# Optimization experiments

Hardware: AMD Instinct MI355X
Metric: run time of the kernel (lower is better)

## Reference

```python
import jax, jax.numpy as jnp
import numpy as np

DIRECTIONS = [(0, 0), (1, 0), (-1, 0), (0, 1), (0, -1)]  # (dx, dy)
BN_EPS = 1e-5


def shift2d(x, directions=DIRECTIONS):
    # x: (B, C, H, W). Split channels into G groups, roll each spatially,
    # zero out the wrapped-around border (zero_pad mode), then concat.
    C = x.shape[1]
    G = len(directions)
    base = C // G
    sizes = [base] * (G - 1) + [C - base * (G - 1)]
    starts = np.concatenate([[0], np.cumsum(sizes)])
    out = []
    for i, (dx, dy) in enumerate(directions):
        chunk = x[:, starts[i]:starts[i + 1]]
        if dx == 0 and dy == 0:
            out.append(chunk)
            continue
        y = jnp.roll(chunk, shift=(dy, dx), axis=(-2, -1))
        if dy > 0:
            y = y.at[..., :dy, :].set(0.0)
        elif dy < 0:
            y = y.at[..., dy:, :].set(0.0)
        if dx > 0:
            y = y.at[..., :, :dx].set(0.0)
        elif dx < 0:
            y = y.at[..., :, dx:].set(0.0)
        out.append(y)
    return jnp.concatenate(out, axis=1)


def setup_inputs() -> dict:
    key = jax.random.key(0)
    k1, k2, k3, k4 = jax.random.split(key, 4)
    B, Cin, Cout, H, W = 32, 256, 256, 56, 56
    x = jax.random.normal(k1, (B, Cin, H, W), dtype=jnp.float32)
    pw_w = jax.random.normal(k2, (Cout, Cin), dtype=jnp.float32) * (1.0 / np.sqrt(Cin))
    gamma = jnp.ones((Cout,), dtype=jnp.float32)
    beta = jnp.zeros((Cout,), dtype=jnp.float32)
    running_mean = jax.random.normal(k3, (Cout,), dtype=jnp.float32) * 0.1
    running_var = jax.random.uniform(k4, (Cout,), dtype=jnp.float32, minval=0.5, maxval=1.5)
    return {"x": x, "pw_w": pw_w, "gamma": gamma, "beta": beta,
            "running_mean": running_mean, "running_var": running_var}


def reference(x, pw_w, gamma, beta, running_mean, running_var):
    # Shift (parameter-free spatial mixing)
    y = shift2d(x)
    # stride=1 -> down is Identity
    # 1x1 conv (no bias): pointwise channel mixing
    y = jnp.einsum('bchw,oc->bohw', y, pw_w)
    # BatchNorm2d (inference form with running stats) + ReLU
    inv = gamma * jax.lax.rsqrt(running_var + BN_EPS)
    y = y * inv[None, :, None, None] + (beta - running_mean * inv)[None, :, None, None]
    return jax.nn.relu(y)
```

## Files before the change

kernel.cpp:

```cpp
#include <hip/hip_runtime.h>

#define H_ 56
#define W_ 56
#define HW_ 3136
#define CIN_ 256
#define COUT_ 256

typedef __attribute__((ext_vector_type(8))) short short8;
typedef __attribute__((ext_vector_type(4))) float f32x4;

__device__ unsigned short g_wbf[COUT_ * CIN_];

__device__ __forceinline__ int swz32(int n) { return ((n ^ (n >> 3)) & 3) << 3; }

__device__ __forceinline__ unsigned short f2bf(float f) {
  union { float f; unsigned int i; } v; v.f = f;
  unsigned int b = v.i + (0x7fffu + ((v.i >> 16) & 1u));
  return (unsigned short)(b >> 16);
}

__device__ __forceinline__ void gload_lds16(const unsigned short* g, unsigned short* l) {
  __builtin_amdgcn_global_load_lds(
      (const __attribute__((address_space(1))) unsigned int*)g,
      (__attribute__((address_space(3))) unsigned int*)l, 16, 0, 0);
}

__device__ __forceinline__ void shift_decode(int c, int& dx, int& dy) {
  if (c < 102)      { dy = 0; dx = (c < 51) ? 0 : 1; }
  else if (c < 153) { dx = -1; dy = 0; }
  else if (c < 204) { dx = 0;  dy = 1; }
  else              { dx = 0;  dy = -1; }
}

__global__ __launch_bounds__(256)
void prep_weights(const float* __restrict__ wgt) {
  int idx  = blockIdx.x * 256 + threadIdx.x;
  int tile = idx >> 12;
  int bm = tile >> 3, kt = tile & 7;
  int e   = idx & 4095;
  int m   = e >> 5, col = e & 31;
  int o   = bm * 128 + m;
  int k   = kt * 32 + (col ^ swz32(m));
  g_wbf[idx] = f2bf(wgt[o * CIN_ + k]);
}

__device__ __forceinline__ void load_x(const float* __restrict__ x, size_t xb,
                                       int hh, int w0, int c,
                                       float4& p0, float4& p1, float& pe) {
  int dx, dy; shift_decode(c, dx, dy);
  int h2 = hh - dy;
  p0 = make_float4(0.f, 0.f, 0.f, 0.f);
  p1 = make_float4(0.f, 0.f, 0.f, 0.f);
  pe = 0.f;
  if ((unsigned)h2 < (unsigned)H_) {
    const float* row = x + xb + (size_t)c * HW_ + h2 * W_;
    p0 = *(const float4*)(row + w0);
    p1 = *(const float4*)(row + w0 + 4);
    if (dx == 1)       { if (w0 > 0)      pe = row[w0 - 1]; }
    else if (dx == -1) { if (w0 + 8 < W_) pe = row[w0 + 8]; }
  }
}

__device__ __forceinline__ void write_b(unsigned short* __restrict__ B,
                                        int nloc0, int krow, int c,
                                        const float4& p0, const float4& p1, float pe) {
  int dx, dy; shift_decode(c, dx, dy);
  float s[8] = {p0.x, p0.y, p0.z, p0.w, p1.x, p1.y, p1.z, p1.w};
  float vals[8];
  if (dx == 0) {
    #pragma unroll
    for (int i = 0; i < 8; ++i) vals[i] = s[i];
  } else if (dx == 1) {
    #pragma unroll
    for (int i = 7; i >= 1; --i) vals[i] = s[i - 1];
    vals[0] = pe;
  } else {
    #pragma unroll
    for (int i = 0; i < 7; ++i) vals[i] = s[i + 1];
    vals[7] = pe;
  }
  #pragma unroll
  for (int i = 0; i < 8; ++i) {
    int nl = nloc0 + i;
    B[nl * 32 + (krow ^ swz32(nl))] = f2bf(vals[i]);
  }
}

__global__ __launch_bounds__(256, 4)
void shiftconv_gemm(const float* __restrict__ x,
                    const float* __restrict__ gamma,
                    const float* __restrict__ beta,
                    const float* __restrict__ rmean,
                    const float* __restrict__ rvar,
                    float* __restrict__ out)
{
  __shared__ unsigned short Alds[2][128 * 32];
  __shared__ unsigned short Blds[2][64 * 32];
  __shared__ float bnp[256];

  const int t    = threadIdx.x;
  const int bn   = blockIdx.x;
  const int bm   = blockIdx.y;
  const int lane = t & 63;
  const int wv   = t >> 6;
  const int wm   = wv >> 1;
  const int wn   = wv & 1;
  const int quad = lane >> 4;
  const int l15  = lane & 15;

  if (t < 128) {
    int o = bm * 128 + t;
    float inv = gamma[o] * rsqrtf(rvar[o] + 1e-5f);
    bnp[2 * t]     = inv;
    bnp[2 * t + 1] = beta[o] - rmean[o] * inv;
  }

  const int chunk  = t & 7;
  const int krow   = t >> 3;
  const int nloc0  = chunk * 8;
  const int nglob0 = bn * 64 + nloc0;
  const int bidx   = nglob0 / HW_;
  const int rem    = nglob0 - bidx * HW_;
  const int hh     = rem / W_;
  const int w0     = rem - hh * W_;
  const size_t xb  = (size_t)bidx * CIN_ * HW_;

  const unsigned short* wsrc = g_wbf + bm * (8 * 4096) + t * 8;

  f32x4 acc[4][2];
  #pragma unroll
  for (int i = 0; i < 4; ++i)
    #pragma unroll
    for (int j = 0; j < 2; ++j)
      acc[i][j] = (f32x4){0.f, 0.f, 0.f, 0.f};

  float4 p0, p1;
  float  pe;

  {
    const unsigned short* g = wsrc;
    gload_lds16(g,        &Alds[0][wv * 512]);
    gload_lds16(g + 2048, &Alds[0][wv * 512 + 2048]);
  }
  load_x(x, xb, hh, w0, krow, p0, p1, pe);
  write_b(&Blds[0][0], nloc0, krow, krow, p0, p1, pe);
  __syncthreads();

  const int kb = quad * 8;
  int buf = 0;

  for (int kt = 0; kt < 8; ++kt) {
    if (kt < 7) {
      const unsigned short* g = wsrc + (kt + 1) * 4096;
      gload_lds16(g,        &Alds[buf ^ 1][wv * 512]);
      gload_lds16(g + 2048, &Alds[buf ^ 1][wv * 512 + 2048]);
      load_x(x, xb, hh, w0, (kt + 1) * 32 + krow, p0, p1, pe);
    }

    short8 af[4], bfr[2];
    #pragma unroll
    for (int f = 0; f < 4; ++f) {
      int ml = wm * 64 + f * 16 + l15;
      af[f] = *(const short8*)(&Alds[buf][ml * 32 + (kb ^ swz32(ml))]);
    }
    #pragma unroll
    for (int g2 = 0; g2 < 2; ++g2) {
      int nl = wn * 32 + g2 * 16 + l15;
      bfr[g2] = *(const short8*)(&Blds[buf][nl * 32 + (kb ^ swz32(nl))]);
    }
    #pragma unroll
    for (int mf = 0; mf < 4; ++mf)
      #pragma unroll
      for (int nf = 0; nf < 2; ++nf)
        acc[mf][nf] = __builtin_amdgcn_mfma_f32_16x16x32_bf16(
            af[mf], bfr[nf], acc[mf][nf], 0, 0, 0);

    if (kt < 7)
      write_b(&Blds[buf ^ 1][0], nloc0, krow, (kt + 1) * 32 + krow, p0, p1, pe);

    __syncthreads();
    buf ^= 1;
  }

  size_t nbase[2];
  #pragma unroll
  for (int nf = 0; nf < 2; ++nf) {
    int ng  = bn * 64 + wn * 32 + nf * 16 + l15;
    int b2  = ng / HW_;
    int hw2 = ng - b2 * HW_;
    nbase[nf] = (size_t)b2 * COUT_ * HW_ + hw2;
  }
  #pragma unroll
  for (int mf = 0; mf < 4; ++mf) {
    int mloc = wm * 64 + mf * 16 + quad * 4;
    float inv[4], add[4];
    #pragma unroll
    for (int r = 0; r < 4; ++r) {
      inv[r] = bnp[2 * (mloc + r)];
      add[r] = bnp[2 * (mloc + r) + 1];
    }
    size_t obase = (size_t)(bm * 128 + mloc) * HW_;
    #pragma unroll
    for (int nf = 0; nf < 2; ++nf) {
      #pragma unroll
      for (int r = 0; r < 4; ++r) {
        float v = fmaf(acc[mf][nf][r], inv[r], add[r]);
        out[nbase[nf] + obase + (size_t)r * HW_] = fmaxf(v, 0.0f);
      }
    }
  }
}

extern "C" void kernel_launch(void* const* d_in, const int* in_sizes, int n_in,
                              void* d_out, int out_size, void* d_ws, size_t ws_size,
                              hipStream_t stream) {
  const float* x     = (const float*)d_in[0];
  const float* wgt   = (const float*)d_in[1];
  const float* gamma = (const float*)d_in[2];
  const float* beta  = (const float*)d_in[3];
  const float* rmean = (const float*)d_in[4];
  const float* rvar  = (const float*)d_in[5];
  float* out = (float*)d_out;

  prep_weights<<<dim3(256), dim3(256), 0, stream>>>(wgt);
  shiftconv_gemm<<<dim3(1568, 2), dim3(256), 0, stream>>>(x, gamma, beta, rmean, rvar, out);
}
```

Before: 211.4 us.

## Prefetch activations two stages ahead, remap blocks across XCDs, raise occupancy

The activation register prefetch becomes two K-stages deep, held in two register slots with a fully unrolled k-loop, so global load latency for x is covered by more MFMA work. The grid is flattened and block IDs are remapped so the two M-halves of an N-tile run adjacently on the same XCD, which improves L2 reuse of x. The occupancy hint rises from 4 to 6 blocks per SM. The extra prefetch registers may conflict with the higher occupancy target and cause spills or a lower real occupancy.

```diff
diff --git a/kernel.cpp b/kernel.cpp
--- a/kernel.cpp
+++ b/kernel.cpp
@@ -86,7 +86,7 @@
   }
 }
 
-__global__ __launch_bounds__(256, 4)
+__global__ __launch_bounds__(256, 6)
 void shiftconv_gemm(const float* __restrict__ x,
                     const float* __restrict__ gamma,
                     const float* __restrict__ beta,
@@ -98,9 +98,12 @@
   __shared__ unsigned short Blds[2][64 * 32];
   __shared__ float bnp[256];
 
-  const int t    = threadIdx.x;
-  const int bn   = blockIdx.x;
-  const int bm   = blockIdx.y;
+  const int t = threadIdx.x;
+  const int orig = blockIdx.x;
+  const int wgid = (orig & 7) * 392 + (orig >> 3);
+  const int bm   = wgid & 1;
+  const int bn   = wgid >> 1;
+
   const int lane = t & 63;
   const int wv   = t >> 6;
   const int wm   = wv >> 1;
@@ -134,28 +137,34 @@
     for (int j = 0; j < 2; ++j)
       acc[i][j] = (f32x4){0.f, 0.f, 0.f, 0.f};
 
-  float4 p0, p1;
-  float  pe;
+  float4 px0[2], px1[2];
+  float  pxe[2];
 
   {
     const unsigned short* g = wsrc;
     gload_lds16(g,        &Alds[0][wv * 512]);
     gload_lds16(g + 2048, &Alds[0][wv * 512 + 2048]);
   }
-  load_x(x, xb, hh, w0, krow, p0, p1, pe);
-  write_b(&Blds[0][0], nloc0, krow, krow, p0, p1, pe);
+  load_x(x, xb, hh, w0, krow, px0[0], px1[0], pxe[0]);
+  write_b(&Blds[0][0], nloc0, krow, krow, px0[0], px1[0], pxe[0]);
+  load_x(x, xb, hh, w0, 32 + krow, px0[1], px1[1], pxe[1]);
   __syncthreads();
 
   const int kb = quad * 8;
-  int buf = 0;
-
+
+  #pragma unroll
   for (int kt = 0; kt < 8; ++kt) {
-    if (kt < 7) {
+    const int buf = kt & 1;
+    const int sW  = (kt + 1) & 1;
+    const int sL  = kt & 1;
+
+    if (kt + 1 < 8) {
       const unsigned short* g = wsrc + (kt + 1) * 4096;
       gload_lds16(g,        &Alds[buf ^ 1][wv * 512]);
       gload_lds16(g + 2048, &Alds[buf ^ 1][wv * 512 + 2048]);
-      load_x(x, xb, hh, w0, (kt + 1) * 32 + krow, p0, p1, pe);
-    }
+    }
+    if (kt + 2 < 8)
+      load_x(x, xb, hh, w0, (kt + 2) * 32 + krow, px0[sL], px1[sL], pxe[sL]);
 
     short8 af[4], bfr[2];
     #pragma unroll
@@ -175,11 +184,11 @@
         acc[mf][nf] = __builtin_amdgcn_mfma_f32_16x16x32_bf16(
             af[mf], bfr[nf], acc[mf][nf], 0, 0, 0);
 
-    if (kt < 7)
-      write_b(&Blds[buf ^ 1][0], nloc0, krow, (kt + 1) * 32 + krow, p0, p1, pe);
+    if (kt + 1 < 8)
+      write_b(&Blds[buf ^ 1][0], nloc0, krow, (kt + 1) * 32 + krow,
+              px0[sW], px1[sW], pxe[sW]);
 
     __syncthreads();
-    buf ^= 1;
   }
 
   size_t nbase[2];
@@ -223,5 +232,5 @@
   float* out = (float*)d_out;
 
   prep_weights<<<dim3(256), dim3(256), 0, stream>>>(wgt);
-  shiftconv_gemm<<<dim3(1568, 2), dim3(256), 0, stream>>>(x, gamma, beta, rmean, rvar, out);
-}
+  shiftconv_gemm<<<dim3(3136), dim3(256), 0, stream>>>(x, gamma, beta, rmean, rvar, out);
+}
```

Measured after the change: 263.8 us. 1.25x slower.
